# Performance work log

Measured on AMD Instinct MI355X. Metric: run time of the kernel, lower is better.

The kernel has to match this reference:

```python
import jax, jax.numpy as jnp
import numpy as np

H = 2048  # hidden_dim


def setup_inputs() -> dict:
    key = jax.random.key(0)
    ks = jax.random.split(key, 10)
    s = 1.0 / np.sqrt(H)
    x = jax.random.normal(ks[0], (4, 2048, H), dtype=jnp.float32)
    Wg = jax.random.uniform(ks[1], (2, H), jnp.float32, -s, s)          # gate weight [2, H]
    W0a = jax.random.uniform(ks[2], (2 * H, H), jnp.float32, -s, s)     # expert0 up
    b0a = jax.random.uniform(ks[3], (2 * H,), jnp.float32, -s, s)
    W0b = jax.random.uniform(ks[4], (H, 2 * H), jnp.float32, -s, s)     # expert0 down
    b0b = jax.random.uniform(ks[5], (H,), jnp.float32, -s, s)
    W1a = jax.random.uniform(ks[6], (2 * H, H), jnp.float32, -s, s)     # expert1 up
    b1a = jax.random.uniform(ks[7], (2 * H,), jnp.float32, -s, s)
    W1b = jax.random.uniform(ks[8], (H, 2 * H), jnp.float32, -s, s)     # expert1 down
    b1b = jax.random.uniform(ks[9], (H,), jnp.float32, -s, s)
    return {"x": x, "Wg": Wg, "W0a": W0a, "b0a": b0a, "W0b": W0b,
            "b0b": b0b, "W1a": W1a, "b1a": b1a, "W1b": W1b, "b1b": b1b}


def reference(x, Wg, W0a, b0a, W0b, b0b, W1a, b1a, W1b, b1b):
    # top-1 gating: softmax over 2 experts, then argmax
    scores = jax.nn.softmax(jnp.einsum('bsh,eh->bse', x, Wg), axis=-1)
    top_expert = jnp.argmax(scores, axis=-1)  # [B, S]
    # expert0: Linear -> GELU (exact, torch default) -> Linear
    h0 = jax.nn.gelu(jnp.einsum('bsh,fh->bsf', x, W0a) + b0a, approximate=False)
    out0 = jnp.einsum('bsf,hf->bsh', h0, W0b) + b0b
    # expert1: Linear -> ReLU -> Linear
    h1 = jax.nn.relu(jnp.einsum('bsh,fh->bsf', x, W1a) + b1a)
    out1 = jnp.einsum('bsf,hf->bsh', h1, W1b) + b1b
    mask0 = (top_expert == 0).astype(x.dtype)[..., None]
    return out0 * mask0 + out1 * (1.0 - mask0)
```

## Files before the change

kernel.cpp:

```cpp
#include <hip/hip_runtime.h>
#include <hip/hip_bf16.h>
#include <math.h>


#define HDIM   2048
#define TOKENS 8192
#define FDIM   4096

typedef __bf16 bf16x8 __attribute__((ext_vector_type(8)));
typedef __bf16 bf16x4 __attribute__((ext_vector_type(4)));
typedef float  f32x4  __attribute__((ext_vector_type(4)));

#define CNT_OFF  0
#define PERM_OFF 256
#define XG_OFF   65536
#define WA_OFF   33619968
#define WB_OFF   67174400
#define HB_OFF   100728832

typedef __attribute__((address_space(1))) const unsigned int as1_u32;
typedef __attribute__((address_space(3))) unsigned int       as3_u32;

__device__ __forceinline__ void gl2lds16(const void* g, void* l) {
    __builtin_amdgcn_global_load_lds((as1_u32*)g, (as3_u32*)l, 16, 0, 0);
}

__global__ void moe_gate_gather(const float* __restrict__ x, const float* __restrict__ Wg,
                                int* __restrict__ n0, int* __restrict__ n1,
                                int* __restrict__ perm, __bf16* __restrict__ Xg) {
    __shared__ int sel[4];
    __shared__ int pos[4];
    const int tid  = threadIdx.x;
    const int wid  = tid >> 6;
    const int lane = tid & 63;
    const int token = blockIdx.x * 4 + wid;
    const float* xr = x + (size_t)token * HDIM;

    float4 xv[8];
    double s0 = 0.0, s1 = 0.0;
#pragma unroll
    for (int j = 0; j < 8; j++) {
        const int idx = j * 256 + lane * 4;
        xv[j] = *reinterpret_cast<const float4*>(xr + idx);
        float4 g0 = *reinterpret_cast<const float4*>(Wg + idx);
        float4 g1 = *reinterpret_cast<const float4*>(Wg + HDIM + idx);
        s0 += (double)xv[j].x * g0.x + (double)xv[j].y * g0.y
            + (double)xv[j].z * g0.z + (double)xv[j].w * g0.w;
        s1 += (double)xv[j].x * g1.x + (double)xv[j].y * g1.y
            + (double)xv[j].z * g1.z + (double)xv[j].w * g1.w;
    }
#pragma unroll
    for (int off = 32; off > 0; off >>= 1) {
        s0 += __shfl_down(s0, off);
        s1 += __shfl_down(s1, off);
    }
    if (lane == 0) sel[wid] = (s1 > s0) ? 1 : 0;
    __syncthreads();
    if (tid == 0) {
        int c0 = (sel[0] == 0) + (sel[1] == 0) + (sel[2] == 0) + (sel[3] == 0);
        int p0 = c0 ? atomicAdd(n0, c0) : 0;
        int p1 = (c0 < 4) ? atomicAdd(n1, 4 - c0) : 0;
#pragma unroll
        for (int w = 0; w < 4; w++) {
            if (sel[w] == 0) pos[w] = p0++;
            else             pos[w] = TOKENS - 1 - (p1++);
        }
    }
    __syncthreads();
    const int dst = pos[wid];
    if (lane == 0) perm[dst] = token;
    __bf16* dr = Xg + (size_t)dst * HDIM;
#pragma unroll
    for (int j = 0; j < 8; j++) {
        const int idx = j * 256 + lane * 4;
        bf16x4 v;
        v[0] = (__bf16)xv[j].x; v[1] = (__bf16)xv[j].y;
        v[2] = (__bf16)xv[j].z; v[3] = (__bf16)xv[j].w;
        *reinterpret_cast<bf16x4*>(dr + idx) = v;
    }
}

__global__ void moe_cast_w(const float* __restrict__ W0a, const float* __restrict__ W1a,
                           const float* __restrict__ W0b, const float* __restrict__ W1b,
                           __bf16* __restrict__ Wa, __bf16* __restrict__ Wb) {
    const int slice = blockIdx.y;
    const float* src;
    __bf16* dst;
    const size_t MS = (size_t)FDIM * HDIM;
    if      (slice == 0) { src = W0a; dst = Wa; }
    else if (slice == 1) { src = W1a; dst = Wa + MS; }
    else if (slice == 2) { src = W0b; dst = Wb; }
    else                 { src = W1b; dst = Wb + MS; }
    const size_t idx = ((size_t)blockIdx.x * 256 + threadIdx.x) * 8;
    float4 a = *reinterpret_cast<const float4*>(src + idx);
    float4 b = *reinterpret_cast<const float4*>(src + idx + 4);
    bf16x8 v;
    v[0] = (__bf16)a.x; v[1] = (__bf16)a.y; v[2] = (__bf16)a.z; v[3] = (__bf16)a.w;
    v[4] = (__bf16)b.x; v[5] = (__bf16)b.y; v[6] = (__bf16)b.z; v[7] = (__bf16)b.w;
    *reinterpret_cast<bf16x8*>(dst + idx) = v;
}

template <int KDIM, int NDIM, bool DOWN>
__global__ void moe_gemm(const __bf16* __restrict__ A, const __bf16* __restrict__ Bw,
                         const float* __restrict__ bias0, const float* __restrict__ bias1,
                         __bf16* __restrict__ Hb, float* __restrict__ Out,
                         const int* __restrict__ n0_ptr, const int* __restrict__ perm) {
    const int e  = blockIdx.z;
    const int n0 = *n0_ptr;
    const int row_lo = e ? n0 : 0;
    const int row_hi = e ? TOKENS : n0;
    const int bm = blockIdx.y * 128;
    if (bm >= row_hi || bm + 128 <= row_lo) return;
    const int bn = blockIdx.x * 128;

    __shared__ __bf16 As[128 * 64];
    __shared__ __bf16 Bs[128 * 64];

    const int tid  = threadIdx.x;
    const int wid  = tid >> 6;
    const int lane = tid & 63;

    const __bf16* Be   = Bw + (size_t)e * NDIM * KDIM;
    const float*  bias = e ? bias1 : bias0;

    const int srow = wid * 32 + (lane >> 3);
    const int skol = (((lane & 7) ^ (lane >> 3)) * 8);
    const __bf16* gA = A  + (size_t)(bm + srow) * KDIM + skol;
    const __bf16* gB = Be + (size_t)(bn + srow) * KDIM + skol;
    __bf16* lA = &As[(wid * 32) * 64];
    __bf16* lB = &Bs[(wid * 32) * 64];

    const int wrow = (wid >> 1) * 64;
    const int wcol = (wid & 1) * 64;
    const int rm = lane & 15;
    const int g  = lane >> 4;
    const int rsw = rm & 7;

    f32x4 acc[4][4] = {};

    for (int kt = 0; kt < KDIM; kt += 64) {
#pragma unroll
        for (int c = 0; c < 4; c++) {
            gl2lds16(gA + (size_t)(c * 8) * KDIM + kt, lA + c * 8 * 64);
            gl2lds16(gB + (size_t)(c * 8) * KDIM + kt, lB + c * 8 * 64);
        }
        __syncthreads();

        bf16x8 aF[2][4], bF[2][4];
#pragma unroll
        for (int h = 0; h < 2; h++) {
            const int csw = ((h * 4 + g) ^ rsw) * 8;
#pragma unroll
            for (int i = 0; i < 4; i++) {
                aF[h][i] = *reinterpret_cast<const bf16x8*>(&As[(wrow + i * 16 + rm) * 64 + csw]);
                bF[h][i] = *reinterpret_cast<const bf16x8*>(&Bs[(wcol + i * 16 + rm) * 64 + csw]);
            }
        }
#pragma unroll
        for (int h = 0; h < 2; h++)
#pragma unroll
            for (int i = 0; i < 4; i++)
#pragma unroll
                for (int j = 0; j < 4; j++)
                    acc[i][j] = __builtin_amdgcn_mfma_f32_16x16x32_bf16(aF[h][i], bF[h][j], acc[i][j], 0, 0, 0);
        __syncthreads();
    }

    const int q4 = g * 4;
#pragma unroll
    for (int j = 0; j < 4; j++) {
        const int col = bn + wcol + j * 16 + rm;
        const float bv = bias[col];
#pragma unroll
        for (int i = 0; i < 4; i++) {
            const int rbase = bm + wrow + i * 16 + q4;
#pragma unroll
            for (int r = 0; r < 4; r++) {
                const int row = rbase + r;
                if (row >= row_lo && row < row_hi) {
                    float v = acc[i][j][r] + bv;
                    if (!DOWN) {
                        if (e == 0) v = 0.5f * v * (1.0f + erff(v * 0.70710678118654752f));
                        else        v = v > 0.0f ? v : 0.0f;
                        Hb[(size_t)row * NDIM + col] = (__bf16)v;
                    } else {
                        Out[(size_t)perm[row] * HDIM + col] = v;
                    }
                }
            }
        }
    }
}

extern "C" void kernel_launch(void* const* d_in, const int* in_sizes, int n_in,
                              void* d_out, int out_size, void* d_ws, size_t ws_size,
                              hipStream_t stream) {
    const float* x   = (const float*)d_in[0];
    const float* Wg  = (const float*)d_in[1];
    const float* W0a = (const float*)d_in[2];
    const float* b0a = (const float*)d_in[3];
    const float* W0b = (const float*)d_in[4];
    const float* b0b = (const float*)d_in[5];
    const float* W1a = (const float*)d_in[6];
    const float* b1a = (const float*)d_in[7];
    const float* W1b = (const float*)d_in[8];
    const float* b1b = (const float*)d_in[9];
    float* out = (float*)d_out;

    char* w = (char*)d_ws;
    int* n0   = (int*)(w + CNT_OFF);
    int* n1   = n0 + 1;
    int* perm = (int*)(w + PERM_OFF);
    __bf16* Xg = (__bf16*)(w + XG_OFF);
    __bf16* Wa = (__bf16*)(w + WA_OFF);
    __bf16* Wb = (__bf16*)(w + WB_OFF);
    __bf16* Hb = (__bf16*)(w + HB_OFF);

    (void)hipMemsetAsync(w, 0, 256, stream);
    moe_gate_gather<<<TOKENS / 4, 256, 0, stream>>>(x, Wg, n0, n1, perm, Xg);
    moe_cast_w<<<dim3(4096, 4), 256, 0, stream>>>(W0a, W1a, W0b, W1b, Wa, Wb);
    moe_gemm<HDIM, FDIM, false><<<dim3(FDIM / 128, TOKENS / 128, 2), 256, 0, stream>>>(
        Xg, Wa, b0a, b1a, Hb, nullptr, n0, perm);
    moe_gemm<FDIM, HDIM, true><<<dim3(HDIM / 128, TOKENS / 128, 2), 256, 0, stream>>>(
        Hb, Wb, b0b, b1b, nullptr, out, n0, perm);
}
```

Measured before the change: 621.6 us.

## Use 256x256 double-buffered 8-wave GEMM with split-K atomics for down projection

```diff
diff --git a/kernel.cpp b/kernel.cpp
--- a/kernel.cpp
+++ b/kernel.cpp
@@ -101,79 +101,151 @@
 }
 
 template <int KDIM, int NDIM, bool DOWN>
-__global__ void moe_gemm(const __bf16* __restrict__ A, const __bf16* __restrict__ Bw,
-                         const float* __restrict__ bias0, const float* __restrict__ bias1,
-                         __bf16* __restrict__ Hb, float* __restrict__ Out,
-                         const int* __restrict__ n0_ptr, const int* __restrict__ perm) {
-    const int e  = blockIdx.z;
+__global__ __launch_bounds__(512, 2) void moe_gemm8(
+        const __bf16* __restrict__ A, const __bf16* __restrict__ Bw,
+        const float* __restrict__ bias0, const float* __restrict__ bias1,
+        __bf16* __restrict__ Hb, float* __restrict__ Out,
+        const int* __restrict__ n0_ptr, const int* __restrict__ perm) {
+    constexpr int KSPAN = DOWN ? KDIM / 2 : KDIM;
+    constexpr int NT    = KSPAN / 64;
+
+    const int z  = blockIdx.z;
+    const int e  = DOWN ? (z >> 1) : z;
+    const int kb = DOWN ? (z & 1)  : 0;
     const int n0 = *n0_ptr;
     const int row_lo = e ? n0 : 0;
     const int row_hi = e ? TOKENS : n0;
-    const int bm = blockIdx.y * 128;
-    if (bm >= row_hi || bm + 128 <= row_lo) return;
-    const int bn = blockIdx.x * 128;
-
-    __shared__ __bf16 As[128 * 64];
-    __shared__ __bf16 Bs[128 * 64];
+    const int bm = blockIdx.y * 256;
+    if (bm >= row_hi || bm + 256 <= row_lo) return;
+    const int bn = blockIdx.x * 256;
+
+    __shared__ __bf16 As[2][256 * 64];
+    __shared__ __bf16 Bs[2][256 * 64];
 
     const int tid  = threadIdx.x;
     const int wid  = tid >> 6;
     const int lane = tid & 63;
+    const int wr   = wid >> 2;
+    const int wc   = wid & 3;
 
     const __bf16* Be   = Bw + (size_t)e * NDIM * KDIM;
     const float*  bias = e ? bias1 : bias0;
 
-    const int srow = wid * 32 + (lane >> 3);
-    const int skol = (((lane & 7) ^ (lane >> 3)) * 8);
-    const __bf16* gA = A  + (size_t)(bm + srow) * KDIM + skol;
-    const __bf16* gB = Be + (size_t)(bn + srow) * KDIM + skol;
-    __bf16* lA = &As[(wid * 32) * 64];
-    __bf16* lB = &Bs[(wid * 32) * 64];
-
-    const int wrow = (wid >> 1) * 64;
-    const int wcol = (wid & 1) * 64;
-    const int rm = lane & 15;
-    const int g  = lane >> 4;
+    const int skol = ((lane & 7) ^ (lane >> 3)) * 8;
+    const __bf16* gA = A  + (size_t)(bm + (wid >> 2) * 128 + (wid & 3) * 16 + (lane >> 3)) * KDIM
+                          + (size_t)kb * KSPAN + skol;
+    const __bf16* gB = Be + (size_t)(bn + wid * 16 + (lane >> 3)) * KDIM
+                          + (size_t)kb * KSPAN + skol;
+    const int al = ((wid >> 2) * 128 + (wid & 3) * 16) * 64;
+    const int bl = (wid * 16) * 64;
+
+    auto stageA = [&](int buf, int rh, int kt) {
+        gl2lds16(gA + (size_t)(rh * 64    ) * KDIM + kt, &As[buf][al + (rh * 64    ) * 64]);
+        gl2lds16(gA + (size_t)(rh * 64 + 8) * KDIM + kt, &As[buf][al + (rh * 64 + 8) * 64]);
+    };
+    auto stageB = [&](int buf, int hb, int kt) {
+        gl2lds16(gB + (size_t)(hb * 128    ) * KDIM + kt, &Bs[buf][bl + (hb * 128    ) * 64]);
+        gl2lds16(gB + (size_t)(hb * 128 + 8) * KDIM + kt, &Bs[buf][bl + (hb * 128 + 8) * 64]);
+    };
+
+    const int rm  = lane & 15;
+    const int g   = lane >> 4;
     const int rsw = rm & 7;
-
-    f32x4 acc[4][4] = {};
-
-    for (int kt = 0; kt < KDIM; kt += 64) {
-#pragma unroll
-        for (int c = 0; c < 4; c++) {
-            gl2lds16(gA + (size_t)(c * 8) * KDIM + kt, lA + c * 8 * 64);
-            gl2lds16(gB + (size_t)(c * 8) * KDIM + kt, lB + c * 8 * 64);
+    const int ra  = (wr * 128 + rm) * 64;
+    const int rb  = (wc * 64  + rm) * 64;
+    const int c0  = ((0 + g) ^ rsw) * 8;
+    const int c1  = ((4 + g) ^ rsw) * 8;
+
+    f32x4  acc[8][4] = {};
+    bf16x8 aF[2][4], bF[2][4];
+
+    auto lda = [&](int buf, int rh, int i2, int kk) {
+        return *reinterpret_cast<const bf16x8*>(
+            &As[buf][ra + (rh * 64 + i2 * 16) * 64 + (kk ? c1 : c0)]);
+    };
+    auto ldb = [&](int buf, int j, int kk) {
+        return *reinterpret_cast<const bf16x8*>(
+            &Bs[buf][rb + j * 16 * 64 + (kk ? c1 : c0)]);
+    };
+    auto mmaQ = [&](int io, int jo) {
+#pragma unroll
+        for (int i2 = 0; i2 < 4; i2++)
+#pragma unroll
+            for (int j = 0; j < 2; j++)
+#pragma unroll
+                for (int kk = 0; kk < 2; kk++)
+                    acc[io + i2][jo + j] = __builtin_amdgcn_mfma_f32_16x16x32_bf16(
+                        aF[kk][i2], bF[kk][jo + j], acc[io + i2][jo + j], 0, 0, 0);
+    };
+
+    stageA(0, 0, 0);  stageA(0, 1, 0);  stageB(0, 0, 0);  stageB(0, 1, 0);
+    stageA(1, 0, 64); stageB(1, 0, 64); stageB(1, 1, 64);
+    asm volatile("s_waitcnt vmcnt(6)" ::: "memory");
+    __builtin_amdgcn_sched_barrier(0);
+    __builtin_amdgcn_s_barrier();
+
+    for (int k = 0; k < NT; ++k) {
+        const int  cur = k & 1;
+        const int  kt1 = (k + 1) * 64;
+        const int  kt2 = (k + 2) * 64;
+        const bool s1  = (k + 1 < NT);
+        const bool s2  = (k + 2 < NT);
+
+#pragma unroll
+        for (int kk = 0; kk < 2; kk++) {
+#pragma unroll
+            for (int i2 = 0; i2 < 4; i2++) aF[kk][i2] = lda(cur, 0, i2, kk);
+#pragma unroll
+            for (int j = 0; j < 2; j++)    bF[kk][j]  = ldb(cur, j, kk);
         }
-        __syncthreads();
-
-        bf16x8 aF[2][4], bF[2][4];
-#pragma unroll
-        for (int h = 0; h < 2; h++) {
-            const int csw = ((h * 4 + g) ^ rsw) * 8;
-#pragma unroll
-            for (int i = 0; i < 4; i++) {
-                aF[h][i] = *reinterpret_cast<const bf16x8*>(&As[(wrow + i * 16 + rm) * 64 + csw]);
-                bF[h][i] = *reinterpret_cast<const bf16x8*>(&Bs[(wcol + i * 16 + rm) * 64 + csw]);
-            }
-        }
-#pragma unroll
-        for (int h = 0; h < 2; h++)
-#pragma unroll
-            for (int i = 0; i < 4; i++)
-#pragma unroll
-                for (int j = 0; j < 4; j++)
-                    acc[i][j] = __builtin_amdgcn_mfma_f32_16x16x32_bf16(aF[h][i], bF[h][j], acc[i][j], 0, 0, 0);
-        __syncthreads();
+        if (s1) stageA(cur ^ 1, 1, kt1);
+        __builtin_amdgcn_s_barrier();
+        __builtin_amdgcn_s_setprio(1);
+        mmaQ(0, 0);
+        __builtin_amdgcn_s_setprio(0);
+        __builtin_amdgcn_s_barrier();
+
+#pragma unroll
+        for (int kk = 0; kk < 2; kk++)
+#pragma unroll
+            for (int j = 0; j < 2; j++) bF[kk][2 + j] = ldb(cur, 2 + j, kk);
+        if (s2) stageA(cur, 0, kt2);
+        __builtin_amdgcn_s_barrier();
+        __builtin_amdgcn_s_setprio(1);
+        mmaQ(0, 2);
+        __builtin_amdgcn_s_setprio(0);
+        __builtin_amdgcn_s_barrier();
+
+#pragma unroll
+        for (int kk = 0; kk < 2; kk++)
+#pragma unroll
+            for (int i2 = 0; i2 < 4; i2++) aF[kk][i2] = lda(cur, 1, i2, kk);
+        if (s2) stageB(cur, 0, kt2);
+        __builtin_amdgcn_s_barrier();
+        __builtin_amdgcn_s_setprio(1);
+        mmaQ(4, 0);
+        __builtin_amdgcn_s_setprio(0);
+        __builtin_amdgcn_s_barrier();
+
+        if (s2) stageB(cur, 1, kt2);
+        __builtin_amdgcn_s_barrier();
+        __builtin_amdgcn_s_setprio(1);
+        mmaQ(4, 2);
+        __builtin_amdgcn_s_setprio(0);
+        if (s2) { asm volatile("s_waitcnt vmcnt(6)" ::: "memory"); }
+        else    { asm volatile("s_waitcnt vmcnt(0)" ::: "memory"); }
+        __builtin_amdgcn_sched_barrier(0);
+        __builtin_amdgcn_s_barrier();
     }
 
     const int q4 = g * 4;
 #pragma unroll
     for (int j = 0; j < 4; j++) {
-        const int col = bn + wcol + j * 16 + rm;
-        const float bv = bias[col];
-#pragma unroll
-        for (int i = 0; i < 4; i++) {
-            const int rbase = bm + wrow + i * 16 + q4;
+        const int col = bn + wc * 64 + j * 16 + rm;
+        const float bv = DOWN ? ((kb == 0) ? bias[col] : 0.0f) : bias[col];
+#pragma unroll
+        for (int i = 0; i < 8; i++) {
+            const int rbase = bm + wr * 128 + i * 16 + q4;
 #pragma unroll
             for (int r = 0; r < 4; r++) {
                 const int row = rbase + r;
@@ -184,7 +256,7 @@
                         else        v = v > 0.0f ? v : 0.0f;
                         Hb[(size_t)row * NDIM + col] = (__bf16)v;
                     } else {
-                        Out[(size_t)perm[row] * HDIM + col] = v;
+                        atomicAdd(Out + (size_t)perm[row] * HDIM + col, v);
                     }
                 }
             }
@@ -217,10 +289,11 @@
     __bf16* Hb = (__bf16*)(w + HB_OFF);
 
     (void)hipMemsetAsync(w, 0, 256, stream);
+    (void)hipMemsetAsync(out, 0, (size_t)TOKENS * HDIM * sizeof(float), stream);
     moe_gate_gather<<<TOKENS / 4, 256, 0, stream>>>(x, Wg, n0, n1, perm, Xg);
     moe_cast_w<<<dim3(4096, 4), 256, 0, stream>>>(W0a, W1a, W0b, W1b, Wa, Wb);
-    moe_gemm<HDIM, FDIM, false><<<dim3(FDIM / 128, TOKENS / 128, 2), 256, 0, stream>>>(
+    moe_gemm8<HDIM, FDIM, false><<<dim3(FDIM / 256, TOKENS / 256, 2), 512, 0, stream>>>(
         Xg, Wa, b0a, b1a, Hb, nullptr, n0, perm);
-    moe_gemm<FDIM, HDIM, true><<<dim3(HDIM / 128, TOKENS / 128, 2), 256, 0, stream>>>(
+    moe_gemm8<FDIM, HDIM, true><<<dim3(HDIM / 256, TOKENS / 256, 4), 512, 0, stream>>>(
         Hb, Wb, b0b, b1b, nullptr, out, n0, perm);
 }
```

New measurement: 852.3 us. 1.37x slower.

## Merge gating and weight-cast kernels; shrink GEMM K-tile from 64 to 32

Applied to the files above, without the earlier changes.

```diff
diff --git a/kernel.cpp b/kernel.cpp
--- a/kernel.cpp
+++ b/kernel.cpp
@@ -25,15 +25,41 @@
     __builtin_amdgcn_global_load_lds((as1_u32*)g, (as3_u32*)l, 16, 0, 0);
 }
 
-__global__ void moe_gate_gather(const float* __restrict__ x, const float* __restrict__ Wg,
-                                int* __restrict__ n0, int* __restrict__ n1,
-                                int* __restrict__ perm, __bf16* __restrict__ Xg) {
+__global__ void moe_prep(const float* __restrict__ x, const float* __restrict__ Wg,
+                         int* __restrict__ n0, int* __restrict__ n1,
+                         int* __restrict__ perm, __bf16* __restrict__ Xg,
+                         const float* __restrict__ W0a, const float* __restrict__ W1a,
+                         const float* __restrict__ W0b, const float* __restrict__ W1b,
+                         __bf16* __restrict__ Wa, __bf16* __restrict__ Wb) {
+    const int bid = blockIdx.x;
+    const int tid = threadIdx.x;
+
+    if (bid >= TOKENS / 4) {
+        const int cid   = bid - TOKENS / 4;
+        const int slice = cid >> 12;
+        const int xblk  = cid & 4095;
+        const float* src;
+        __bf16* dst;
+        const size_t MS = (size_t)FDIM * HDIM;
+        if      (slice == 0) { src = W0a; dst = Wa; }
+        else if (slice == 1) { src = W1a; dst = Wa + MS; }
+        else if (slice == 2) { src = W0b; dst = Wb; }
+        else                 { src = W1b; dst = Wb + MS; }
+        const size_t idx = ((size_t)xblk * 256 + tid) * 8;
+        float4 a = *reinterpret_cast<const float4*>(src + idx);
+        float4 b = *reinterpret_cast<const float4*>(src + idx + 4);
+        bf16x8 v;
+        v[0] = (__bf16)a.x; v[1] = (__bf16)a.y; v[2] = (__bf16)a.z; v[3] = (__bf16)a.w;
+        v[4] = (__bf16)b.x; v[5] = (__bf16)b.y; v[6] = (__bf16)b.z; v[7] = (__bf16)b.w;
+        *reinterpret_cast<bf16x8*>(dst + idx) = v;
+        return;
+    }
+
     __shared__ int sel[4];
     __shared__ int pos[4];
-    const int tid  = threadIdx.x;
     const int wid  = tid >> 6;
     const int lane = tid & 63;
-    const int token = blockIdx.x * 4 + wid;
+    const int token = bid * 4 + wid;
     const float* xr = x + (size_t)token * HDIM;
 
     float4 xv[8];
@@ -78,26 +104,6 @@
         v[2] = (__bf16)xv[j].z; v[3] = (__bf16)xv[j].w;
         *reinterpret_cast<bf16x4*>(dr + idx) = v;
     }
-}
-
-__global__ void moe_cast_w(const float* __restrict__ W0a, const float* __restrict__ W1a,
-                           const float* __restrict__ W0b, const float* __restrict__ W1b,
-                           __bf16* __restrict__ Wa, __bf16* __restrict__ Wb) {
-    const int slice = blockIdx.y;
-    const float* src;
-    __bf16* dst;
-    const size_t MS = (size_t)FDIM * HDIM;
-    if      (slice == 0) { src = W0a; dst = Wa; }
-    else if (slice == 1) { src = W1a; dst = Wa + MS; }
-    else if (slice == 2) { src = W0b; dst = Wb; }
-    else                 { src = W1b; dst = Wb + MS; }
-    const size_t idx = ((size_t)blockIdx.x * 256 + threadIdx.x) * 8;
-    float4 a = *reinterpret_cast<const float4*>(src + idx);
-    float4 b = *reinterpret_cast<const float4*>(src + idx + 4);
-    bf16x8 v;
-    v[0] = (__bf16)a.x; v[1] = (__bf16)a.y; v[2] = (__bf16)a.z; v[3] = (__bf16)a.w;
-    v[4] = (__bf16)b.x; v[5] = (__bf16)b.y; v[6] = (__bf16)b.z; v[7] = (__bf16)b.w;
-    *reinterpret_cast<bf16x8*>(dst + idx) = v;
 }
 
 template <int KDIM, int NDIM, bool DOWN>
@@ -113,8 +119,8 @@
     if (bm >= row_hi || bm + 128 <= row_lo) return;
     const int bn = blockIdx.x * 128;
 
-    __shared__ __bf16 As[128 * 64];
-    __shared__ __bf16 Bs[128 * 64];
+    __shared__ __bf16 As[128 * 32];
+    __shared__ __bf16 Bs[128 * 32];
 
     const int tid  = threadIdx.x;
     const int wid  = tid >> 6;
@@ -123,46 +129,41 @@
     const __bf16* Be   = Bw + (size_t)e * NDIM * KDIM;
     const float*  bias = e ? bias1 : bias0;
 
-    const int srow = wid * 32 + (lane >> 3);
-    const int skol = (((lane & 7) ^ (lane >> 3)) * 8);
+    const int srow = wid * 32 + (lane >> 2);
+    const int skol = (((lane & 3) ^ ((lane >> 2) & 3)) * 8);
     const __bf16* gA = A  + (size_t)(bm + srow) * KDIM + skol;
     const __bf16* gB = Be + (size_t)(bn + srow) * KDIM + skol;
-    __bf16* lA = &As[(wid * 32) * 64];
-    __bf16* lB = &Bs[(wid * 32) * 64];
+    __bf16* lA = &As[(wid * 32) * 32];
+    __bf16* lB = &Bs[(wid * 32) * 32];
 
     const int wrow = (wid >> 1) * 64;
     const int wcol = (wid & 1) * 64;
     const int rm = lane & 15;
     const int g  = lane >> 4;
-    const int rsw = rm & 7;
+    const int rsw = rm & 3;
 
     f32x4 acc[4][4] = {};
 
-    for (int kt = 0; kt < KDIM; kt += 64) {
-#pragma unroll
-        for (int c = 0; c < 4; c++) {
-            gl2lds16(gA + (size_t)(c * 8) * KDIM + kt, lA + c * 8 * 64);
-            gl2lds16(gB + (size_t)(c * 8) * KDIM + kt, lB + c * 8 * 64);
+    for (int kt = 0; kt < KDIM; kt += 32) {
+#pragma unroll
+        for (int c = 0; c < 2; c++) {
+            gl2lds16(gA + (size_t)(c * 16) * KDIM + kt, lA + c * 16 * 32);
+            gl2lds16(gB + (size_t)(c * 16) * KDIM + kt, lB + c * 16 * 32);
         }
         __syncthreads();
 
-        bf16x8 aF[2][4], bF[2][4];
-#pragma unroll
-        for (int h = 0; h < 2; h++) {
-            const int csw = ((h * 4 + g) ^ rsw) * 8;
-#pragma unroll
-            for (int i = 0; i < 4; i++) {
-                aF[h][i] = *reinterpret_cast<const bf16x8*>(&As[(wrow + i * 16 + rm) * 64 + csw]);
-                bF[h][i] = *reinterpret_cast<const bf16x8*>(&Bs[(wcol + i * 16 + rm) * 64 + csw]);
-            }
-        }
-#pragma unroll
-        for (int h = 0; h < 2; h++)
-#pragma unroll
-            for (int i = 0; i < 4; i++)
-#pragma unroll
-                for (int j = 0; j < 4; j++)
-                    acc[i][j] = __builtin_amdgcn_mfma_f32_16x16x32_bf16(aF[h][i], bF[h][j], acc[i][j], 0, 0, 0);
+        const int csw = (g ^ rsw) * 8;
+        bf16x8 aF[4], bF[4];
+#pragma unroll
+        for (int i = 0; i < 4; i++) {
+            aF[i] = *reinterpret_cast<const bf16x8*>(&As[(wrow + i * 16 + rm) * 32 + csw]);
+            bF[i] = *reinterpret_cast<const bf16x8*>(&Bs[(wcol + i * 16 + rm) * 32 + csw]);
+        }
+#pragma unroll
+        for (int i = 0; i < 4; i++)
+#pragma unroll
+            for (int j = 0; j < 4; j++)
+                acc[i][j] = __builtin_amdgcn_mfma_f32_16x16x32_bf16(aF[i], bF[j], acc[i][j], 0, 0, 0);
         __syncthreads();
     }
 
@@ -217,8 +218,8 @@
     __bf16* Hb = (__bf16*)(w + HB_OFF);
 
     (void)hipMemsetAsync(w, 0, 256, stream);
-    moe_gate_gather<<<TOKENS / 4, 256, 0, stream>>>(x, Wg, n0, n1, perm, Xg);
-    moe_cast_w<<<dim3(4096, 4), 256, 0, stream>>>(W0a, W1a, W0b, W1b, Wa, Wb);
+    moe_prep<<<TOKENS / 4 + 4 * 4096, 256, 0, stream>>>(
+        x, Wg, n0, n1, perm, Xg, W0a, W1a, W0b, W1b, Wa, Wb);
     moe_gemm<HDIM, FDIM, false><<<dim3(FDIM / 128, TOKENS / 128, 2), 256, 0, stream>>>(
         Xg, Wa, b0a, b1a, Hb, nullptr, n0, perm);
     moe_gemm<FDIM, HDIM, true><<<dim3(HDIM / 128, TOKENS / 128, 2), 256, 0, stream>>>(
```

Result: slower. 682.1 us (+9.7%).
